# Kernel tuning notes

Measured on AMD Instinct MI355X. Metric: run time of the kernel, lower is better.

## Reference

```python
import jax, jax.numpy as jnp
import numpy as np

NEG_W = 0.5  # negative_weight

def setup_inputs() -> dict:
    key = jax.random.key(0)
    ks = jax.random.split(key, 11)
    U, V, P, F, D, NF = 16384, 50000, 65536, 20, 64, 100000
    return {
        "user_emb": jax.random.normal(ks[0], (NF, D), jnp.float32),
        "item_emb": jax.random.normal(ks[1], (NF, D), jnp.float32),
        "w_user": jax.random.normal(ks[2], (NF,), jnp.float32),
        "w_item": jax.random.normal(ks[3], (NF,), jnp.float32),
        "bias": jax.random.normal(ks[4], (1,), jnp.float32),
        "h1": jax.random.normal(ks[5], (D,), jnp.float32),
        "h2": jax.random.normal(ks[6], (D,), jnp.float32),
        "user_feat_idx": jax.random.randint(ks[7], (U, F), 0, NF, jnp.int32),
        "item_feat_idx": jax.random.randint(ks[8], (V, F), 0, NF, jnp.int32),
        "pos_user_ids": jax.random.randint(ks[9], (P,), 0, U, jnp.int32),
        "pos_item_ids": jax.random.randint(ks[10], (P,), 0, V, jnp.int32),
    }

def _entity_terms(emb, w, feat_idx, h1, extra):
    # emb: [NF,D], feat_idx: [N,F] -> batched gather + FM bi-interaction
    g = emb[feat_idx]                      # [N,F,D]
    s = g.sum(axis=1)                      # [N,D]  (p_ud / q_vd)
    bi = 0.5 * (jnp.square(s) - jnp.square(g).sum(axis=1))  # [N,D]
    scalar = bi @ h1 + w[feat_idx].sum(axis=1) + extra       # [N]
    return s, scalar

def reference(user_emb, item_emb, w_user, w_item, bias, h1, h2,
              user_feat_idx, item_feat_idx, pos_user_ids, pos_item_ids):
    U = user_feat_idx.shape[0]
    V = item_feat_idx.shape[0]
    ones_u = jnp.ones((U, 1), user_emb.dtype)
    ones_v = jnp.ones((V, 1), item_emb.dtype)

    p_ud, su = _entity_terms(user_emb, w_user, user_feat_idx, h1, bias[0])
    q_vd, sv = _entity_terms(item_emb, w_item, item_feat_idx, h1, 0.0)
    p_u = jnp.concatenate([p_ud, su[:, None], ones_u], axis=1)  # [U,D+2]
    q_v = jnp.concatenate([q_vd, ones_v, sv[:, None]], axis=1)  # [V,D+2]

    # negative (all-pairs) term via D x D Gram matrices
    A = p_ud.T @ p_ud                                           # [D,D]
    B = q_vd.T @ q_vd                                           # [D,D]
    loss_neg = NEG_W * jnp.einsum('i,j,ij,ij->', h2, h2, A, B)

    # positive-pair term
    hv = jnp.concatenate([h2, jnp.ones((2,), h2.dtype)])        # [D+2]
    y = jnp.einsum('pd,pd,d->p', p_u[pos_user_ids], q_v[pos_item_ids], hv)
    loss_pos = jnp.sum((1.0 - NEG_W) * jnp.square(y) - 2.0 * y)

    return jnp.reshape(loss_neg + loss_pos, (1,))
```

## Files before the change

kernel.cpp:

```cpp
#include <hip/hip_runtime.h>

#define FD 20
#define DD 64

#define GA 64
#define GB 128
#define GAB 16
#define GBB 32
#define POSB 2048
#define NEGB 64

typedef float float4v __attribute__((ext_vector_type(4)));
typedef unsigned short ushort4v __attribute__((ext_vector_type(4)));
typedef unsigned short ushort8v __attribute__((ext_vector_type(8)));
typedef short short8v __attribute__((ext_vector_type(8)));

__device__ __forceinline__ unsigned short f2bf(float f) {
    unsigned u = __float_as_uint(f);
    unsigned r = u + 0x7fffu + ((u >> 16) & 1u);
    return (unsigned short)(r >> 16);
}
__device__ __forceinline__ float bf2f(unsigned short h) {
    return __uint_as_float((unsigned)h << 16);
}

__global__ __launch_bounds__(256) void conv_kernel(
    const float* __restrict__ ue, const float* __restrict__ ie,
    unsigned int* __restrict__ u8, unsigned int* __restrict__ i8,
    int n4, float* __restrict__ out, int out_size)
{
    int i = blockIdx.x * blockDim.x + threadIdx.x;
    if (i < out_size) out[i] = 0.0f;
    if (i >= 2 * n4) return;
    const float4v* src; unsigned int* dst; int k;
    if (i < n4) { src = (const float4v*)ue; dst = u8; k = i; }
    else        { src = (const float4v*)ie; dst = i8; k = i - n4; }
    float4v v = src[k];
    unsigned int p = 0;
    p = __builtin_amdgcn_cvt_pk_fp8_f32(v.x, v.y, p, false);
    p = __builtin_amdgcn_cvt_pk_fp8_f32(v.z, v.w, p, true);
    dst[k] = p;
}

__global__ __launch_bounds__(256, 4) void entity_kernel(
    const unsigned char* __restrict__ user_f8,
    const unsigned char* __restrict__ item_f8,
    const float* __restrict__ w_user, const float* __restrict__ w_item,
    const float* __restrict__ bias, const float* __restrict__ h1,
    const int* __restrict__ ufeat, const int* __restrict__ ifeat,
    unsigned short* __restrict__ p_bf, float* __restrict__ su,
    unsigned short* __restrict__ q_bf, float* __restrict__ sv,
    int U, int V)
{
    int wid  = (int)((blockIdx.x * blockDim.x + threadIdx.x) >> 6);
    int lane = threadIdx.x & 63;
    if (wid >= U + V) return;

    const unsigned char* emb; const float* wv; const int* fidx; float extra;
    unsigned short* srow; float* sc;
    if (wid < U) {
        emb = user_f8; wv = w_user; fidx = ufeat + (size_t)wid * FD;
        extra = bias[0]; srow = p_bf + (size_t)wid * DD; sc = su + wid;
    } else {
        int m = wid - U;
        emb = item_f8; wv = w_item; fidx = ifeat + (size_t)m * FD;
        extra = 0.0f; srow = q_bf + (size_t)m * DD; sc = sv + m;
    }

    int myidx = 0; float myw = 0.0f;
    if (lane < FD) {
        myidx = fidx[lane];
        myw   = wv[myidx];
    }

    int grp = lane >> 4;
    int c   = lane & 15;

    int fx[5];
#pragma unroll
    for (int i = 0; i < 5; ++i)
        fx[i] = __shfl(myidx, grp + 4 * i, 64);

    unsigned int hw[5];
#pragma unroll
    for (int i = 0; i < 5; ++i)
        hw[i] = *((const unsigned int*)(emb + (size_t)fx[i] * DD) + c);

    float4v s4 = (float4v)0.0f, ss4 = (float4v)0.0f;
#pragma unroll
    for (int i = 0; i < 5; ++i) {
        float4v g;
        g.x = __builtin_amdgcn_cvt_f32_fp8(hw[i], 0);
        g.y = __builtin_amdgcn_cvt_f32_fp8(hw[i], 1);
        g.z = __builtin_amdgcn_cvt_f32_fp8(hw[i], 2);
        g.w = __builtin_amdgcn_cvt_f32_fp8(hw[i], 3);
        s4 += g; ss4 += g * g;
    }

#pragma unroll
    for (int off = 16; off <= 32; off <<= 1) {
        float4v t, u;
        t.x = __shfl_xor(s4.x,  off, 64); t.y = __shfl_xor(s4.y,  off, 64);
        t.z = __shfl_xor(s4.z,  off, 64); t.w = __shfl_xor(s4.w,  off, 64);
        u.x = __shfl_xor(ss4.x, off, 64); u.y = __shfl_xor(ss4.y, off, 64);
        u.z = __shfl_xor(ss4.z, off, 64); u.w = __shfl_xor(ss4.w, off, 64);
        s4 += t; ss4 += u;
    }

    float part = myw;
    if (grp == 0) {
        float4v h14 = *(const float4v*)(h1 + c * 4);
        float4v bi4 = 0.5f * (s4 * s4 - ss4);
        part += bi4.x*h14.x + bi4.y*h14.y + bi4.z*h14.z + bi4.w*h14.w;
        ushort4v o;
        o.x = f2bf(s4.x); o.y = f2bf(s4.y); o.z = f2bf(s4.z); o.w = f2bf(s4.w);
        *(ushort4v*)(srow + c * 4) = o;
    }

#pragma unroll
    for (int off = 1; off <= 32; off <<= 1)
        part += __shfl_xor(part, off, 64);

    if (lane == 0) *sc = part + extra;
}

__device__ __forceinline__ void gram_block_mfma(
    const unsigned short* __restrict__ M, int nrows, int gwid, int nw,
    float* __restrict__ Gpart)
{
    int lane = threadIdx.x & 63;
    int q = lane >> 4;
    int c = lane & 15;

    float4v acc[4][4];
#pragma unroll
    for (int ti = 0; ti < 4; ++ti)
#pragma unroll
        for (int tj = 0; tj < 4; ++tj)
            acc[ti][tj] = (float4v)0.0f;

    int ntiles = (nrows + 63) >> 6;
    for (int tt = gwid; tt < ntiles; tt += nw) {
        int row0 = tt << 6;
#pragma unroll
        for (int kb = 0; kb < 2; ++kb) {
            int r0 = row0 + kb * 32 + q * 8;
            const unsigned short* base = M + (size_t)r0 * DD + c;
            short8v f[4];
            if (row0 + 64 <= nrows) {
#pragma unroll
                for (int Db = 0; Db < 4; ++Db)
#pragma unroll
                    for (int j = 0; j < 8; ++j)
                        f[Db][j] = (short)base[(size_t)j * DD + Db * 16];
            } else {
#pragma unroll
                for (int Db = 0; Db < 4; ++Db)
#pragma unroll
                    for (int j = 0; j < 8; ++j)
                        f[Db][j] = (r0 + j < nrows)
                                 ? (short)base[(size_t)j * DD + Db * 16]
                                 : (short)0;
            }
#pragma unroll
            for (int ti = 0; ti < 4; ++ti)
#pragma unroll
                for (int tj = 0; tj < 4; ++tj)
                    acc[ti][tj] = __builtin_amdgcn_mfma_f32_16x16x32_bf16(
                        f[ti], f[tj], acc[ti][tj], 0, 0, 0);
        }
    }

    float* out = Gpart + (size_t)gwid * (DD * DD);
#pragma unroll
    for (int ti = 0; ti < 4; ++ti)
#pragma unroll
        for (int tj = 0; tj < 4; ++tj)
#pragma unroll
            for (int rg = 0; rg < 4; ++rg)
                out[(ti * 16 + q * 4 + rg) * DD + tj * 16 + c] = acc[ti][tj][rg];
}

__global__ __launch_bounds__(256) void mid_kernel(
    const unsigned short* __restrict__ p_bf, int U, float* __restrict__ PA,
    const unsigned short* __restrict__ q_bf, int V, float* __restrict__ PB,
    const float* __restrict__ su, const float* __restrict__ sv,
    const float* __restrict__ h2,
    const int* __restrict__ pu, const int* __restrict__ pi,
    int P, float* __restrict__ posPart)
{
    __shared__ float red[4];
    int w = threadIdx.x >> 6;

    if (blockIdx.x < GAB) {
        gram_block_mfma(p_bf, U, blockIdx.x * 4 + w, GA, PA);
        return;
    }
    if (blockIdx.x < GAB + GBB) {
        gram_block_mfma(q_bf, V, (blockIdx.x - GAB) * 4 + w, GB, PB);
        return;
    }

    int lane = threadIdx.x & 63;
    int sl   = lane & 15;
    int sub  = lane >> 4;
    int pb   = blockIdx.x - (GAB + GBB);
    int wId  = pb * 4 + w;
    const int NW = POSB * 4;

    float4v h2v = *(const float4v*)(h2 + sl * 4);

    int pid0 = wId * 4 + sub;
    int pid1 = pid0 + NW * 4;
    bool ok0 = pid0 < P, ok1 = pid1 < P;

    int u0 = 0, v0 = 0, u1 = 0, v1 = 0;
    if (ok0) { u0 = pu[pid0]; v0 = pi[pid0]; }
    if (ok1) { u1 = pu[pid1]; v1 = pi[pid1]; }

    ushort4v ph0 = (ushort4v)0, qh0 = (ushort4v)0;
    ushort4v ph1 = (ushort4v)0, qh1 = (ushort4v)0;
    if (ok0) {
        ph0 = *(const ushort4v*)(p_bf + (size_t)u0 * DD + sl * 4);
        qh0 = *(const ushort4v*)(q_bf + (size_t)v0 * DD + sl * 4);
    }
    if (ok1) {
        ph1 = *(const ushort4v*)(p_bf + (size_t)u1 * DD + sl * 4);
        qh1 = *(const ushort4v*)(q_bf + (size_t)v1 * DD + sl * 4);
    }

    float d0 = bf2f(ph0.x)*bf2f(qh0.x)*h2v.x + bf2f(ph0.y)*bf2f(qh0.y)*h2v.y
             + bf2f(ph0.z)*bf2f(qh0.z)*h2v.z + bf2f(ph0.w)*bf2f(qh0.w)*h2v.w;
    float d1 = bf2f(ph1.x)*bf2f(qh1.x)*h2v.x + bf2f(ph1.y)*bf2f(qh1.y)*h2v.y
             + bf2f(ph1.z)*bf2f(qh1.z)*h2v.z + bf2f(ph1.w)*bf2f(qh1.w)*h2v.w;
#pragma unroll
    for (int off = 1; off < 16; off <<= 1) {
        d0 += __shfl_xor(d0, off, 64);
        d1 += __shfl_xor(d1, off, 64);
    }

    float acc = 0.0f;
    if (sl == 0) {
        if (ok0) { float y = d0 + su[u0] + sv[v0]; acc += 0.5f * y * y - 2.0f * y; }
        if (ok1) { float y = d1 + su[u1] + sv[v1]; acc += 0.5f * y * y - 2.0f * y; }
    }
    acc += __shfl_xor(acc, 16, 64);
    acc += __shfl_xor(acc, 32, 64);
    if (lane == 0) red[w] = acc;
    __syncthreads();
    if (threadIdx.x == 0)
        posPart[pb] = red[0] + red[1] + red[2] + red[3];
}

__global__ __launch_bounds__(256) void neg_reduce_kernel(
    const float* __restrict__ PA, const float* __restrict__ PB,
    const float* __restrict__ h2, const float* __restrict__ posPart,
    float* __restrict__ out)
{
    __shared__ float sA[4][64], sB[4][64];
    __shared__ float sPos;
    int t  = threadIdx.x;
    int l  = t & 63;
    int ch = t >> 6;
    int e  = blockIdx.x * 64 + l;

    float a = 0.0f, b = 0.0f;
#pragma unroll
    for (int k = 0; k < GA / 4; ++k)
        a += PA[(size_t)(ch * (GA / 4) + k) * (DD * DD) + e];
#pragma unroll
    for (int k = 0; k < GB / 4; ++k)
        b += PB[(size_t)(ch * (GB / 4) + k) * (DD * DD) + e];
    sA[ch][l] = a;
    sB[ch][l] = b;

    if (ch == 1) {
        float p = (l < POSB / NEGB) ? posPart[blockIdx.x * (POSB / NEGB) + l] : 0.0f;
#pragma unroll
        for (int off = 1; off <= 32; off <<= 1)
            p += __shfl_xor(p, off, 64);
        if (l == 0) sPos = p;
    }
    __syncthreads();

    if (ch == 0) {
        float fa = sA[0][l] + sA[1][l] + sA[2][l] + sA[3][l];
        float fb = sB[0][l] + sB[1][l] + sB[2][l] + sB[3][l];
        float acc = 0.5f * h2[blockIdx.x] * h2[l] * fa * fb;
#pragma unroll
        for (int off = 1; off <= 32; off <<= 1)
            acc += __shfl_xor(acc, off, 64);
        if (l == 0)
            atomicAdd(out, acc + sPos);
    }
}

extern "C" void kernel_launch(void* const* d_in, const int* in_sizes, int n_in,
                              void* d_out, int out_size, void* d_ws, size_t ws_size,
                              hipStream_t stream)
{
    const float* user_emb = (const float*)d_in[0];
    const float* item_emb = (const float*)d_in[1];
    const float* w_user   = (const float*)d_in[2];
    const float* w_item   = (const float*)d_in[3];
    const float* bias     = (const float*)d_in[4];
    const float* h1       = (const float*)d_in[5];
    const float* h2       = (const float*)d_in[6];
    const int*   ufeat    = (const int*)d_in[7];
    const int*   ifeat    = (const int*)d_in[8];
    const int*   pu       = (const int*)d_in[9];
    const int*   pi       = (const int*)d_in[10];

    const int NF = in_sizes[0] / DD;
    const int U  = in_sizes[7] / FD;
    const int V  = in_sizes[8] / FD;
    const int P  = in_sizes[9];

    float* ws = (float*)d_ws;
    size_t off = 0;
    unsigned short* p_bf = (unsigned short*)(ws + off); off += (size_t)U * DD / 2;
    unsigned short* q_bf = (unsigned short*)(ws + off); off += (size_t)V * DD / 2;
    float* su   = ws + off; off += (size_t)U;          off = (off + 63) & ~(size_t)63;
    float* sv   = ws + off; off += (size_t)V;          off = (off + 63) & ~(size_t)63;
    float* PA   = ws + off; off += (size_t)GA * DD * DD;
    float* PB   = ws + off; off += (size_t)GB * DD * DD;
    float* posPart = ws + off; off += (size_t)POSB;    off = (off + 63) & ~(size_t)63;
    unsigned char* uf8 = (unsigned char*)(ws + off);   off += (size_t)NF * DD / 4;
    unsigned char* if8 = (unsigned char*)(ws + off);   off += (size_t)NF * DD / 4;

    float* out = (float*)d_out;

    int n4 = NF * DD / 4;
    conv_kernel<<<(2 * n4 + 255) / 256, 256, 0, stream>>>(
        user_emb, item_emb, (unsigned int*)uf8, (unsigned int*)if8,
        n4, out, out_size);

    int nent = U + V;
    entity_kernel<<<(nent + 3) / 4, 256, 0, stream>>>(
        uf8, if8, w_user, w_item, bias, h1,
        ufeat, ifeat, p_bf, su, q_bf, sv, U, V);

    mid_kernel<<<GAB + GBB + POSB, 256, 0, stream>>>(
        p_bf, U, PA, q_bf, V, PB, su, sv, h2, pu, pi, P, posPart);

    neg_reduce_kernel<<<NEGB, 256, 0, stream>>>(PA, PB, h2, posPart, out);
}
```

Measured before the change: 148.5 us.

## Process four entities per wavefront with 16 lanes each in entity kernel

The entity kernel now assigns each 16-lane group its own entity, so each lane loads all 20 feature indices and gathers 20 fp8 words itself. Previously a whole wave handled one entity and split the features across lanes. This removes the cross-group shuffle reduction and quarters the number of waves launched. The fp8 decode also moves to the packed two-wide conversion builtin. In exchange each lane uses more registers and issues redundant index loads across its 16 lanes, which may lower occupancy.

```diff
diff --git a/kernel.cpp b/kernel.cpp
--- a/kernel.cpp
+++ b/kernel.cpp
@@ -10,6 +10,7 @@
 #define POSB 2048
 #define NEGB 64
 
+typedef float float2v __attribute__((ext_vector_type(2)));
 typedef float float4v __attribute__((ext_vector_type(4)));
 typedef unsigned short ushort4v __attribute__((ext_vector_type(4)));
 typedef unsigned short ushort8v __attribute__((ext_vector_type(8)));
@@ -52,76 +53,57 @@
     unsigned short* __restrict__ q_bf, float* __restrict__ sv,
     int U, int V)
 {
-    int wid  = (int)((blockIdx.x * blockDim.x + threadIdx.x) >> 6);
+    int gwid = (int)((blockIdx.x * blockDim.x + threadIdx.x) >> 6);
     int lane = threadIdx.x & 63;
-    if (wid >= U + V) return;
-
-    const unsigned char* emb; const float* wv; const int* fidx; float extra;
-    unsigned short* srow; float* sc;
-    if (wid < U) {
-        emb = user_f8; wv = w_user; fidx = ufeat + (size_t)wid * FD;
-        extra = bias[0]; srow = p_bf + (size_t)wid * DD; sc = su + wid;
-    } else {
-        int m = wid - U;
-        emb = item_f8; wv = w_item; fidx = ifeat + (size_t)m * FD;
-        extra = 0.0f; srow = q_bf + (size_t)m * DD; sc = sv + m;
-    }
-
-    int myidx = 0; float myw = 0.0f;
-    if (lane < FD) {
-        myidx = fidx[lane];
-        myw   = wv[myidx];
-    }
-
-    int grp = lane >> 4;
-    int c   = lane & 15;
-
-    int fx[5];
-#pragma unroll
-    for (int i = 0; i < 5; ++i)
-        fx[i] = __shfl(myidx, grp + 4 * i, 64);
-
-    unsigned int hw[5];
-#pragma unroll
-    for (int i = 0; i < 5; ++i)
-        hw[i] = *((const unsigned int*)(emb + (size_t)fx[i] * DD) + c);
+    int eg   = lane >> 4;
+    int c    = lane & 15;
+    int ent  = gwid * 4 + eg;
+    if (ent >= U + V) return;
+
+    bool isU = ent < U;
+    int  m   = isU ? ent : ent - U;
+    const unsigned char* emb = isU ? user_f8 : item_f8;
+    const float* wv   = isU ? w_user : w_item;
+    const int*   fidx = (isU ? ufeat : ifeat) + (size_t)m * FD;
+    float extra       = isU ? bias[0] : 0.0f;
+    unsigned short* srow = (isU ? p_bf : q_bf) + (size_t)m * DD;
+    float* sc         = (isU ? su : sv) + m;
+
+    int idx[FD];
+#pragma unroll
+    for (int j = 0; j < FD; ++j) idx[j] = fidx[j];
+
+    unsigned int hw[FD];
+#pragma unroll
+    for (int j = 0; j < FD; ++j)
+        hw[j] = *((const unsigned int*)(emb + (size_t)idx[j] * DD) + c);
 
     float4v s4 = (float4v)0.0f, ss4 = (float4v)0.0f;
 #pragma unroll
-    for (int i = 0; i < 5; ++i) {
+    for (int j = 0; j < FD; ++j) {
+        float2v lo = __builtin_amdgcn_cvt_pk_f32_fp8(hw[j], false);
+        float2v hi = __builtin_amdgcn_cvt_pk_f32_fp8(hw[j], true);
         float4v g;
-        g.x = __builtin_amdgcn_cvt_f32_fp8(hw[i], 0);
-        g.y = __builtin_amdgcn_cvt_f32_fp8(hw[i], 1);
-        g.z = __builtin_amdgcn_cvt_f32_fp8(hw[i], 2);
-        g.w = __builtin_amdgcn_cvt_f32_fp8(hw[i], 3);
+        g.x = lo.x; g.y = lo.y; g.z = hi.x; g.w = hi.y;
         s4 += g; ss4 += g * g;
     }
 
-#pragma unroll
-    for (int off = 16; off <= 32; off <<= 1) {
-        float4v t, u;
-        t.x = __shfl_xor(s4.x,  off, 64); t.y = __shfl_xor(s4.y,  off, 64);
-        t.z = __shfl_xor(s4.z,  off, 64); t.w = __shfl_xor(s4.w,  off, 64);
-        u.x = __shfl_xor(ss4.x, off, 64); u.y = __shfl_xor(ss4.y, off, 64);
-        u.z = __shfl_xor(ss4.z, off, 64); u.w = __shfl_xor(ss4.w, off, 64);
-        s4 += t; ss4 += u;
-    }
-
-    float part = myw;
-    if (grp == 0) {
-        float4v h14 = *(const float4v*)(h1 + c * 4);
-        float4v bi4 = 0.5f * (s4 * s4 - ss4);
-        part += bi4.x*h14.x + bi4.y*h14.y + bi4.z*h14.z + bi4.w*h14.w;
-        ushort4v o;
-        o.x = f2bf(s4.x); o.y = f2bf(s4.y); o.z = f2bf(s4.z); o.w = f2bf(s4.w);
-        *(ushort4v*)(srow + c * 4) = o;
-    }
-
-#pragma unroll
-    for (int off = 1; off <= 32; off <<= 1)
+    float part = wv[idx[c]];
+    if (c < FD - 16) part += wv[idx[16 + c]];
+
+    float4v h14 = *(const float4v*)(h1 + c * 4);
+    float4v bi4 = 0.5f * (s4 * s4 - ss4);
+    part += bi4.x*h14.x + bi4.y*h14.y + bi4.z*h14.z + bi4.w*h14.w;
+
+#pragma unroll
+    for (int off = 1; off <= 8; off <<= 1)
         part += __shfl_xor(part, off, 64);
 
-    if (lane == 0) *sc = part + extra;
+    ushort4v o;
+    o.x = f2bf(s4.x); o.y = f2bf(s4.y); o.z = f2bf(s4.z); o.w = f2bf(s4.w);
+    *(ushort4v*)(srow + c * 4) = o;
+
+    if (c == 0) *sc = part + extra;
 }
 
 __device__ __forceinline__ void gram_block_mfma(
@@ -336,7 +318,8 @@
         n4, out, out_size);
 
     int nent = U + V;
-    entity_kernel<<<(nent + 3) / 4, 256, 0, stream>>>(
+    int nwaves = (nent + 3) / 4;
+    entity_kernel<<<(nwaves + 3) / 4, 256, 0, stream>>>(
         uf8, if8, w_user, w_item, bias, h1,
         ufeat, ifeat, p_bf, su, q_bf, sv, U, V);
 
```

Result: faster. 144.4 us, median of 2 (-2.7%).
